# Kernel tuning notes

Measured on AMD Instinct MI355X. Metric: run time of the kernel, lower is better.

The kernel has to match this reference:

```python
import jax, jax.numpy as jnp
import numpy as np

NUM_USERS = 100_000
NUM_ITEMS = 50_000
D = 64           # input_dim
K = 3            # num_weights (basis diagonal weights)
C = 5            # num_classes
E = 2_000_000    # number of (user, item) edges


def setup_inputs() -> dict:
    key = jax.random.key(0)
    ks = jax.random.split(key, 8)
    he = np.sqrt(2.0 / D).astype(np.float32)  # he_normal scale for [*, D] weights
    return {
        "u_feat": jax.random.normal(ks[0], (NUM_USERS, D), dtype=jnp.float32),
        "v_feat": jax.random.normal(ks[1], (NUM_ITEMS, D), dtype=jnp.float32),
        "W": jax.random.normal(ks[2], (K, D), dtype=jnp.float32) * he,
        "scalars": jax.random.normal(ks[3], (K, C), dtype=jnp.float32) * np.sqrt(2.0 / K).astype(np.float32),
        "u_bias": jnp.zeros((NUM_USERS, C), dtype=jnp.float32) + 0.01 * jax.random.normal(ks[4], (NUM_USERS, C), dtype=jnp.float32),
        "v_bias": jnp.zeros((NUM_ITEMS, C), dtype=jnp.float32) + 0.01 * jax.random.normal(ks[5], (NUM_ITEMS, C), dtype=jnp.float32),
        "u_idx": jax.random.randint(ks[6], (E,), 0, NUM_USERS, dtype=jnp.int32),
        "v_idx": jax.random.randint(ks[7], (E,), 0, NUM_ITEMS, dtype=jnp.int32),
    }


def reference(u_feat, v_feat, W, scalars, u_bias, v_bias, u_idx, v_idx):
    # Gather per-edge user/item embedding rows: [E, D]
    u_g = u_feat[u_idx]
    v_g = v_feat[v_idx]
    # Diagonal bilinear form per basis k: sum_d u_d * W[k,d] * v_d
    # = (u * v) @ W^T  -> basis_outputs: [E, K]
    basis_outputs = (u_g * v_g) @ W.T
    # Combine bases into class logits: [E, C]
    outputs = basis_outputs @ scalars
    # user_item_bias=True: add gathered per-user / per-item class biases
    outputs = outputs + u_bias[u_idx] + v_bias[v_idx]
    # activation=None -> linear
    return outputs
```

## Files before the change

### kernel.cpp

```cpp
#include <hip/hip_runtime.h>
#include <hip/hip_fp16.h>


__global__ __launch_bounds__(256) void convert_tables_fp16(
    const float* __restrict__ u_feat, const float* __restrict__ v_feat,
    __half* __restrict__ u_h, __half* __restrict__ v_h, int nu, int nv)
{
    const int tid  = blockIdx.x * blockDim.x + threadIdx.x;
    const int nthr = gridDim.x * blockDim.x;
    for (int i = tid * 4; i < nu; i += nthr * 4) {
        const float4 x = *reinterpret_cast<const float4*>(u_feat + i);
        *reinterpret_cast<__half2*>(u_h + i)     = __floats2half2_rn(x.x, x.y);
        *reinterpret_cast<__half2*>(u_h + i + 2) = __floats2half2_rn(x.z, x.w);
    }
    for (int i = tid * 4; i < nv; i += nthr * 4) {
        const float4 x = *reinterpret_cast<const float4*>(v_feat + i);
        *reinterpret_cast<__half2*>(v_h + i)     = __floats2half2_rn(x.x, x.y);
        *reinterpret_cast<__half2*>(v_h + i + 2) = __floats2half2_rn(x.z, x.w);
    }
}

__global__ __launch_bounds__(256) void bilinear_edges_h(
    const __half* __restrict__ u_h, const __half* __restrict__ v_h,
    const float* __restrict__ W, const float* __restrict__ scalars,
    const float* __restrict__ u_bias, const float* __restrict__ v_bias,
    const int* __restrict__ u_idx, const int* __restrict__ v_idx,
    float* __restrict__ out, int E)
{
    const int tid    = blockIdx.x * blockDim.x + threadIdx.x;
    const int sl     = threadIdx.x & 15;
    const int group  = tid >> 4;
    const int ngroup = (gridDim.x * blockDim.x) >> 4;

    const int d0 = sl * 4;
    float m[4][5];
    {
        float w0[4], w1[4], w2[4];
        #pragma unroll
        for (int j = 0; j < 4; ++j) {
            w0[j] = W[0 * 64 + d0 + j];
            w1[j] = W[1 * 64 + d0 + j];
            w2[j] = W[2 * 64 + d0 + j];
        }
        #pragma unroll
        for (int c = 0; c < 5; ++c) {
            const float s0 = scalars[0 * 5 + c];
            const float s1 = scalars[1 * 5 + c];
            const float s2 = scalars[2 * 5 + c];
            #pragma unroll
            for (int j = 0; j < 4; ++j)
                m[j][c] = w0[j] * s0 + w1[j] * s1 + w2[j] * s2;
        }
    }

    for (int e0 = group * 2; e0 < E; e0 += ngroup * 2) {
        const int  e1   = e0 + 1;
        const bool has1 = (e1 < E);

        const int uu0 = u_idx[e0];
        const int vv0 = v_idx[e0];
        const int uu1 = has1 ? u_idx[e1] : uu0;
        const int vv1 = has1 ? v_idx[e1] : vv0;

        const float2 ur0 = *reinterpret_cast<const float2*>(u_h + (size_t)uu0 * 64 + d0);
        const float2 vr0 = *reinterpret_cast<const float2*>(v_h + (size_t)vv0 * 64 + d0);
        const float2 ur1 = *reinterpret_cast<const float2*>(u_h + (size_t)uu1 * 64 + d0);
        const float2 vr1 = *reinterpret_cast<const float2*>(v_h + (size_t)vv1 * 64 + d0);

        float ub0 = 0.f, vb0 = 0.f, ub1 = 0.f, vb1 = 0.f;
        if (sl < 5) {
            ub0 = u_bias[(size_t)uu0 * 5 + sl];
            vb0 = v_bias[(size_t)vv0 * 5 + sl];
            ub1 = u_bias[(size_t)uu1 * 5 + sl];
            vb1 = v_bias[(size_t)vv1 * 5 + sl];
        }

        const float2 u0a = __half22float2(*reinterpret_cast<const __half2*>(&ur0.x));
        const float2 u0b = __half22float2(*reinterpret_cast<const __half2*>(&ur0.y));
        const float2 v0a = __half22float2(*reinterpret_cast<const __half2*>(&vr0.x));
        const float2 v0b = __half22float2(*reinterpret_cast<const __half2*>(&vr0.y));
        const float2 u1a = __half22float2(*reinterpret_cast<const __half2*>(&ur1.x));
        const float2 u1b = __half22float2(*reinterpret_cast<const __half2*>(&ur1.y));
        const float2 v1a = __half22float2(*reinterpret_cast<const __half2*>(&vr1.x));
        const float2 v1b = __half22float2(*reinterpret_cast<const __half2*>(&vr1.y));

        const float a0 = u0a.x * v0a.x, a1 = u0a.y * v0a.y,
                    a2 = u0b.x * v0b.x, a3 = u0b.y * v0b.y;
        const float b0 = u1a.x * v1a.x, b1 = u1a.y * v1a.y,
                    b2 = u1b.x * v1b.x, b3 = u1b.y * v1b.y;

        float accA[5], accB[5];
        #pragma unroll
        for (int c = 0; c < 5; ++c) {
            accA[c] = a0 * m[0][c] + a1 * m[1][c] + a2 * m[2][c] + a3 * m[3][c];
            accB[c] = b0 * m[0][c] + b1 * m[1][c] + b2 * m[2][c] + b3 * m[3][c];
        }

        #pragma unroll
        for (int mask = 1; mask < 16; mask <<= 1) {
            #pragma unroll
            for (int c = 0; c < 5; ++c) {
                accA[c] += __shfl_xor(accA[c], mask, 64);
                accB[c] += __shfl_xor(accB[c], mask, 64);
            }
        }

        if (sl < 5) {
            out[(size_t)e0 * 5 + sl] = accA[sl] + ub0 + vb0;
            if (has1)
                out[(size_t)e1 * 5 + sl] = accB[sl] + ub1 + vb1;
        }
    }
}

__global__ __launch_bounds__(256) void bilinear_edges_f32(
    const float* __restrict__ u_feat, const float* __restrict__ v_feat,
    const float* __restrict__ W, const float* __restrict__ scalars,
    const float* __restrict__ u_bias, const float* __restrict__ v_bias,
    const int* __restrict__ u_idx, const int* __restrict__ v_idx,
    float* __restrict__ out, int E)
{
    const int tid    = blockIdx.x * blockDim.x + threadIdx.x;
    const int sl     = threadIdx.x & 15;
    const int group  = tid >> 4;
    const int ngroup = (gridDim.x * blockDim.x) >> 4;

    const int d0 = sl * 4;
    float m[4][5];
    {
        float w0[4], w1[4], w2[4];
        #pragma unroll
        for (int j = 0; j < 4; ++j) {
            w0[j] = W[0 * 64 + d0 + j];
            w1[j] = W[1 * 64 + d0 + j];
            w2[j] = W[2 * 64 + d0 + j];
        }
        #pragma unroll
        for (int c = 0; c < 5; ++c) {
            const float s0 = scalars[0 * 5 + c];
            const float s1 = scalars[1 * 5 + c];
            const float s2 = scalars[2 * 5 + c];
            #pragma unroll
            for (int j = 0; j < 4; ++j)
                m[j][c] = w0[j] * s0 + w1[j] * s1 + w2[j] * s2;
        }
    }

    for (int e0 = group * 2; e0 < E; e0 += ngroup * 2) {
        const int  e1   = e0 + 1;
        const bool has1 = (e1 < E);
        const int uu0 = u_idx[e0];
        const int vv0 = v_idx[e0];
        const int uu1 = has1 ? u_idx[e1] : uu0;
        const int vv1 = has1 ? v_idx[e1] : vv0;

        const float4 u40 = *reinterpret_cast<const float4*>(u_feat + (size_t)uu0 * 64 + d0);
        const float4 v40 = *reinterpret_cast<const float4*>(v_feat + (size_t)vv0 * 64 + d0);
        const float4 u41 = *reinterpret_cast<const float4*>(u_feat + (size_t)uu1 * 64 + d0);
        const float4 v41 = *reinterpret_cast<const float4*>(v_feat + (size_t)vv1 * 64 + d0);

        float ub0 = 0.f, vb0 = 0.f, ub1 = 0.f, vb1 = 0.f;
        if (sl < 5) {
            ub0 = u_bias[(size_t)uu0 * 5 + sl];
            vb0 = v_bias[(size_t)vv0 * 5 + sl];
            ub1 = u_bias[(size_t)uu1 * 5 + sl];
            vb1 = v_bias[(size_t)vv1 * 5 + sl];
        }

        const float a0 = u40.x * v40.x, a1 = u40.y * v40.y,
                    a2 = u40.z * v40.z, a3 = u40.w * v40.w;
        const float b0 = u41.x * v41.x, b1 = u41.y * v41.y,
                    b2 = u41.z * v41.z, b3 = u41.w * v41.w;

        float accA[5], accB[5];
        #pragma unroll
        for (int c = 0; c < 5; ++c) {
            accA[c] = a0 * m[0][c] + a1 * m[1][c] + a2 * m[2][c] + a3 * m[3][c];
            accB[c] = b0 * m[0][c] + b1 * m[1][c] + b2 * m[2][c] + b3 * m[3][c];
        }
        #pragma unroll
        for (int mask = 1; mask < 16; mask <<= 1) {
            #pragma unroll
            for (int c = 0; c < 5; ++c) {
                accA[c] += __shfl_xor(accA[c], mask, 64);
                accB[c] += __shfl_xor(accB[c], mask, 64);
            }
        }
        if (sl < 5) {
            out[(size_t)e0 * 5 + sl] = accA[sl] + ub0 + vb0;
            if (has1)
                out[(size_t)e1 * 5 + sl] = accB[sl] + ub1 + vb1;
        }
    }
}

extern "C" void kernel_launch(void* const* d_in, const int* in_sizes, int n_in,
                              void* d_out, int out_size, void* d_ws, size_t ws_size,
                              hipStream_t stream) {
    const float* u_feat  = (const float*)d_in[0];
    const float* v_feat  = (const float*)d_in[1];
    const float* W       = (const float*)d_in[2];
    const float* scalars = (const float*)d_in[3];
    const float* u_bias  = (const float*)d_in[4];
    const float* v_bias  = (const float*)d_in[5];
    const int*   u_idx   = (const int*)d_in[6];
    const int*   v_idx   = (const int*)d_in[7];
    float*       out     = (float*)d_out;

    const int nu = in_sizes[0];
    const int nv = in_sizes[1];
    const int E  = in_sizes[6];

    const size_t ws_need = (size_t)(nu + nv) * sizeof(__half);

    if (ws_size >= ws_need) {
        __half* u_h = (__half*)d_ws;
        __half* v_h = u_h + nu;
        convert_tables_fp16<<<2048, 256, 0, stream>>>(u_feat, v_feat, u_h, v_h, nu, nv);
        bilinear_edges_h<<<2048, 256, 0, stream>>>(
            u_h, v_h, W, scalars, u_bias, v_bias, u_idx, v_idx, out, E);
    } else {
        bilinear_edges_f32<<<2048, 256, 0, stream>>>(
            u_feat, v_feat, W, scalars, u_bias, v_bias, u_idx, v_idx, out, E);
    }
}
```

Before: 243.6 us.

## Reduce three basis sums with DPP and prefetch next edge indices

The per-edge reduction now sums the three basis projections across 16 lanes instead of five folded class logits, and applies the 3x5 scalar mix only on the output lanes. The xor shuffles are replaced by DPP row operations (quad_perm and row_shr), so each step adds a cross-lane move to the value. The fp16 kernel also loads the next iteration's index pair early to hide index-load latency, and the fp32 fallback is simplified to one edge per iteration. This cuts cross-lane traffic from 10 to 6 values per edge pair. The row_shr pattern leaves the full sum only in lane 15 of each row, so the outputs read from lanes 0-4 may be incomplete.

```diff
diff --git a/kernel.cpp b/kernel.cpp
--- a/kernel.cpp
+++ b/kernel.cpp
@@ -1,6 +1,19 @@
 #include <hip/hip_runtime.h>
 #include <hip/hip_fp16.h>
 
+
+template <int CTRL>
+__device__ __forceinline__ float dpp_add(float x) {
+    int t = __builtin_amdgcn_update_dpp(0, __float_as_int(x), CTRL, 0xF, 0xF, true);
+    return x + __int_as_float(t);
+}
+
+__device__ __forceinline__ void reduce16_3(float& a, float& b, float& c) {
+    a = dpp_add<0xB1>(a);  b = dpp_add<0xB1>(b);  c = dpp_add<0xB1>(c);
+    a = dpp_add<0x4E>(a);  b = dpp_add<0x4E>(b);  c = dpp_add<0x4E>(c);
+    a = dpp_add<0x124>(a); b = dpp_add<0x124>(b); c = dpp_add<0x124>(c);
+    a = dpp_add<0x128>(a); b = dpp_add<0x128>(b); c = dpp_add<0x128>(c);
+}
 
 __global__ __launch_bounds__(256) void convert_tables_fp16(
     const float* __restrict__ u_feat, const float* __restrict__ v_feat,
@@ -31,48 +44,52 @@
     const int sl     = threadIdx.x & 15;
     const int group  = tid >> 4;
     const int ngroup = (gridDim.x * blockDim.x) >> 4;
+    const int step   = ngroup * 2;
 
     const int d0 = sl * 4;
-    float m[4][5];
-    {
-        float w0[4], w1[4], w2[4];
-        #pragma unroll
-        for (int j = 0; j < 4; ++j) {
-            w0[j] = W[0 * 64 + d0 + j];
-            w1[j] = W[1 * 64 + d0 + j];
-            w2[j] = W[2 * 64 + d0 + j];
-        }
-        #pragma unroll
-        for (int c = 0; c < 5; ++c) {
-            const float s0 = scalars[0 * 5 + c];
-            const float s1 = scalars[1 * 5 + c];
-            const float s2 = scalars[2 * 5 + c];
-            #pragma unroll
-            for (int j = 0; j < 4; ++j)
-                m[j][c] = w0[j] * s0 + w1[j] * s1 + w2[j] * s2;
-        }
+    float w0[4], w1[4], w2[4];
+    #pragma unroll
+    for (int j = 0; j < 4; ++j) {
+        w0[j] = W[0 * 64 + d0 + j];
+        w1[j] = W[1 * 64 + d0 + j];
+        w2[j] = W[2 * 64 + d0 + j];
     }
+    float s0 = 0.f, s1 = 0.f, s2 = 0.f;
+    if (sl < 5) { s0 = scalars[0 * 5 + sl]; s1 = scalars[1 * 5 + sl]; s2 = scalars[2 * 5 + sl]; }
 
-    for (int e0 = group * 2; e0 < E; e0 += ngroup * 2) {
+    int e0 = group * 2;
+    if (e0 >= E) return;
+
+    int uu0 = u_idx[e0];
+    int vv0 = v_idx[e0];
+    int uu1 = (e0 + 1 < E) ? u_idx[e0 + 1] : uu0;
+    int vv1 = (e0 + 1 < E) ? v_idx[e0 + 1] : vv0;
+
+    for (; e0 < E; e0 += step) {
         const int  e1   = e0 + 1;
         const bool has1 = (e1 < E);
+        const int cu0 = uu0, cv0 = vv0, cu1 = uu1, cv1 = vv1;
 
-        const int uu0 = u_idx[e0];
-        const int vv0 = v_idx[e0];
-        const int uu1 = has1 ? u_idx[e1] : uu0;
-        const int vv1 = has1 ? v_idx[e1] : vv0;
+        const float2 ur0 = *reinterpret_cast<const float2*>(u_h + (size_t)cu0 * 64 + d0);
+        const float2 vr0 = *reinterpret_cast<const float2*>(v_h + (size_t)cv0 * 64 + d0);
+        const float2 ur1 = *reinterpret_cast<const float2*>(u_h + (size_t)cu1 * 64 + d0);
+        const float2 vr1 = *reinterpret_cast<const float2*>(v_h + (size_t)cv1 * 64 + d0);
 
-        const float2 ur0 = *reinterpret_cast<const float2*>(u_h + (size_t)uu0 * 64 + d0);
-        const float2 vr0 = *reinterpret_cast<const float2*>(v_h + (size_t)vv0 * 64 + d0);
-        const float2 ur1 = *reinterpret_cast<const float2*>(u_h + (size_t)uu1 * 64 + d0);
-        const float2 vr1 = *reinterpret_cast<const float2*>(v_h + (size_t)vv1 * 64 + d0);
+        const int en = e0 + step;
+        if (en < E) {
+            uu0 = u_idx[en];
+            vv0 = v_idx[en];
+            const int en1 = en + 1;
+            uu1 = (en1 < E) ? u_idx[en1] : uu0;
+            vv1 = (en1 < E) ? v_idx[en1] : vv0;
+        }
 
         float ub0 = 0.f, vb0 = 0.f, ub1 = 0.f, vb1 = 0.f;
         if (sl < 5) {
-            ub0 = u_bias[(size_t)uu0 * 5 + sl];
-            vb0 = v_bias[(size_t)vv0 * 5 + sl];
-            ub1 = u_bias[(size_t)uu1 * 5 + sl];
-            vb1 = v_bias[(size_t)vv1 * 5 + sl];
+            ub0 = u_bias[(size_t)cu0 * 5 + sl];
+            vb0 = v_bias[(size_t)cv0 * 5 + sl];
+            ub1 = u_bias[(size_t)cu1 * 5 + sl];
+            vb1 = v_bias[(size_t)cv1 * 5 + sl];
         }
 
         const float2 u0a = __half22float2(*reinterpret_cast<const __half2*>(&ur0.x));
@@ -89,26 +106,20 @@
         const float b0 = u1a.x * v1a.x, b1 = u1a.y * v1a.y,
                     b2 = u1b.x * v1b.x, b3 = u1b.y * v1b.y;
 
-        float accA[5], accB[5];
-        #pragma unroll
-        for (int c = 0; c < 5; ++c) {
-            accA[c] = a0 * m[0][c] + a1 * m[1][c] + a2 * m[2][c] + a3 * m[3][c];
-            accB[c] = b0 * m[0][c] + b1 * m[1][c] + b2 * m[2][c] + b3 * m[3][c];
-        }
+        float qa0 = a0*w0[0] + a1*w0[1] + a2*w0[2] + a3*w0[3];
+        float qa1 = a0*w1[0] + a1*w1[1] + a2*w1[2] + a3*w1[3];
+        float qa2 = a0*w2[0] + a1*w2[1] + a2*w2[2] + a3*w2[3];
+        float qb0 = b0*w0[0] + b1*w0[1] + b2*w0[2] + b3*w0[3];
+        float qb1 = b0*w1[0] + b1*w1[1] + b2*w1[2] + b3*w1[3];
+        float qb2 = b0*w2[0] + b1*w2[1] + b2*w2[2] + b3*w2[3];
 
-        #pragma unroll
-        for (int mask = 1; mask < 16; mask <<= 1) {
-            #pragma unroll
-            for (int c = 0; c < 5; ++c) {
-                accA[c] += __shfl_xor(accA[c], mask, 64);
-                accB[c] += __shfl_xor(accB[c], mask, 64);
-            }
-        }
+        reduce16_3(qa0, qa1, qa2);
+        reduce16_3(qb0, qb1, qb2);
 
         if (sl < 5) {
-            out[(size_t)e0 * 5 + sl] = accA[sl] + ub0 + vb0;
+            out[(size_t)e0 * 5 + sl] = qa0 * s0 + qa1 * s1 + qa2 * s2 + ub0 + vb0;
             if (has1)
-                out[(size_t)e1 * 5 + sl] = accB[sl] + ub1 + vb1;
+                out[(size_t)e1 * 5 + sl] = qb0 * s0 + qb1 * s1 + qb2 * s2 + ub1 + vb1;
         }
     }
 }
@@ -126,71 +137,32 @@
     const int ngroup = (gridDim.x * blockDim.x) >> 4;
 
     const int d0 = sl * 4;
-    float m[4][5];
-    {
-        float w0[4], w1[4], w2[4];
-        #pragma unroll
-        for (int j = 0; j < 4; ++j) {
-            w0[j] = W[0 * 64 + d0 + j];
-            w1[j] = W[1 * 64 + d0 + j];
-            w2[j] = W[2 * 64 + d0 + j];
-        }
-        #pragma unroll
-        for (int c = 0; c < 5; ++c) {
-            const float s0 = scalars[0 * 5 + c];
-            const float s1 = scalars[1 * 5 + c];
-            const float s2 = scalars[2 * 5 + c];
-            #pragma unroll
-            for (int j = 0; j < 4; ++j)
-                m[j][c] = w0[j] * s0 + w1[j] * s1 + w2[j] * s2;
-        }
+    float w0[4], w1[4], w2[4];
+    #pragma unroll
+    for (int j = 0; j < 4; ++j) {
+        w0[j] = W[0 * 64 + d0 + j];
+        w1[j] = W[1 * 64 + d0 + j];
+        w2[j] = W[2 * 64 + d0 + j];
     }
+    float s0 = 0.f, s1 = 0.f, s2 = 0.f;
+    if (sl < 5) { s0 = scalars[0 * 5 + sl]; s1 = scalars[1 * 5 + sl]; s2 = scalars[2 * 5 + sl]; }
 
-    for (int e0 = group * 2; e0 < E; e0 += ngroup * 2) {
-        const int  e1   = e0 + 1;
-        const bool has1 = (e1 < E);
-        const int uu0 = u_idx[e0];
-        const int vv0 = v_idx[e0];
-        const int uu1 = has1 ? u_idx[e1] : uu0;
-        const int vv1 = has1 ? v_idx[e1] : vv0;
+    for (int e = group; e < E; e += ngroup) {
+        const int uu = u_idx[e];
+        const int vv = v_idx[e];
+        const float4 u4 = *reinterpret_cast<const float4*>(u_feat + (size_t)uu * 64 + d0);
+        const float4 v4 = *reinterpret_cast<const float4*>(v_feat + (size_t)vv * 64 + d0);
+        float ub = 0.f, vb = 0.f;
+        if (sl < 5) { ub = u_bias[(size_t)uu * 5 + sl]; vb = v_bias[(size_t)vv * 5 + sl]; }
 
-        const float4 u40 = *reinterpret_cast<const float4*>(u_feat + (size_t)uu0 * 64 + d0);
-        const float4 v40 = *reinterpret_cast<const float4*>(v_feat + (size_t)vv0 * 64 + d0);
-        const float4 u41 = *reinterpret_cast<const float4*>(u_feat + (size_t)uu1 * 64 + d0);
-        const float4 v41 = *reinterpret_cast<const float4*>(v_feat + (size_t)vv1 * 64 + d0);
-
-        float ub0 = 0.f, vb0 = 0.f, ub1 = 0.f, vb1 = 0.f;
-        if (sl < 5) {
-            ub0 = u_bias[(size_t)uu0 * 5 + sl];
-            vb0 = v_bias[(size_t)vv0 * 5 + sl];
-            ub1 = u_bias[(size_t)uu1 * 5 + sl];
-            vb1 = v_bias[(size_t)vv1 * 5 + sl];
-        }
-
-        const float a0 = u40.x * v40.x, a1 = u40.y * v40.y,
-                    a2 = u40.z * v40.z, a3 = u40.w * v40.w;
-        const float b0 = u41.x * v41.x, b1 = u41.y * v41.y,
-                    b2 = u41.z * v41.z, b3 = u41.w * v41.w;
-
-        float accA[5], accB[5];
-        #pragma unroll
-        for (int c = 0; c < 5; ++c) {
-            accA[c] = a0 * m[0][c] + a1 * m[1][c] + a2 * m[2][c] + a3 * m[3][c];
-            accB[c] = b0 * m[0][c] + b1 * m[1][c] + b2 * m[2][c] + b3 * m[3][c];
-        }
-        #pragma unroll
-        for (int mask = 1; mask < 16; mask <<= 1) {
-            #pragma unroll
-            for (int c = 0; c < 5; ++c) {
-                accA[c] += __shfl_xor(accA[c], mask, 64);
-                accB[c] += __shfl_xor(accB[c], mask, 64);
-            }
-        }
-        if (sl < 5) {
-            out[(size_t)e0 * 5 + sl] = accA[sl] + ub0 + vb0;
-            if (has1)
-                out[(size_t)e1 * 5 + sl] = accB[sl] + ub1 + vb1;
-        }
+        const float p0 = u4.x * v4.x, p1 = u4.y * v4.y,
+                    p2 = u4.z * v4.z, p3 = u4.w * v4.w;
+        float q0 = p0*w0[0] + p1*w0[1] + p2*w0[2] + p3*w0[3];
+        float q1 = p0*w1[0] + p1*w1[1] + p2*w1[2] + p3*w1[3];
+        float q2 = p0*w2[0] + p1*w2[1] + p2*w2[2] + p3*w2[3];
+        reduce16_3(q0, q1, q2);
+        if (sl < 5)
+            out[(size_t)e * 5 + sl] = q0 * s0 + q1 * s1 + q2 * s2 + ub + vb;
     }
 }
 
```

New measurement: 208.0 us. 1.17x faster.
